# Performance work log

Measured on AMD Instinct MI355X. Metric: run time of the kernel, lower is better.

Reference implementation:

```python
import jax, jax.numpy as jnp
import numpy as np

EPS = 1e-5
GROUPS = 32


def setup_inputs() -> dict:
    key = jax.random.key(0)
    ks = jax.random.split(key, 3)
    B, C, H, W = 4, 256, 64, 64
    x = jax.random.normal(ks[0], (B, C, H, W), dtype=jnp.float32)
    gn_w = jnp.ones((C,), dtype=jnp.float32)
    gn_b = jnp.zeros((C,), dtype=jnp.float32)
    qkv_w = jax.random.normal(ks[1], (3 * C, C), dtype=jnp.float32) * (C ** -0.5)
    qkv_b = jnp.zeros((3 * C,), dtype=jnp.float32)
    proj_w = jax.random.normal(ks[2], (C, C), dtype=jnp.float32) * (C ** -0.5)
    proj_b = jnp.zeros((C,), dtype=jnp.float32)
    return {"x": x, "gn_w": gn_w, "gn_b": gn_b, "qkv_w": qkv_w,
            "qkv_b": qkv_b, "proj_w": proj_w, "proj_b": proj_b}


def reference(x, gn_w, gn_b, qkv_w, qkv_b, proj_w, proj_b):
    B, C, H, W = x.shape
    N = H * W
    # GroupNorm over (C//G, H, W) per group
    xg = x.reshape(B, GROUPS, -1)
    mean = xg.mean(axis=-1, keepdims=True)
    var = xg.var(axis=-1, keepdims=True)
    h = ((xg - mean) * jax.lax.rsqrt(var + EPS)).reshape(B, C, H, W)
    h = h * gn_w[None, :, None, None] + gn_b[None, :, None, None]
    # 1x1 conv QKV == channel GEMM
    hf = h.reshape(B, C, N)
    qkv = jnp.einsum('oc,bcn->bon', qkv_w, hf) + qkv_b[None, :, None]
    q, k, v = (qkv[:, :C], qkv[:, C:2 * C], qkv[:, 2 * C:])  # each [B,C,N]
    scale = C ** -0.5
    attn = jax.nn.softmax(jnp.einsum('bcn,bcm->bnm', q, k) * scale, axis=-1)
    out = jnp.einsum('bnm,bcm->bcn', attn, v)  # [B,C,N]
    y = jnp.einsum('oc,bcn->bon', proj_w, out) + proj_b[None, :, None]
    return x + y.reshape(B, C, H, W)
```

## Files before the change

kernel.cpp:

```cpp
#include <hip/hip_runtime.h>
#include <cstdint>
#include <cstddef>

typedef __attribute__((ext_vector_type(8))) short bf16x8;
typedef __attribute__((ext_vector_type(4))) short s16x4;
typedef __attribute__((ext_vector_type(2))) short s16x2;
typedef __attribute__((ext_vector_type(4))) float f32x4;
typedef __attribute__((ext_vector_type(16))) float f32x16;
typedef __attribute__((ext_vector_type(4))) unsigned u32x4;

#define DEVI static __device__ __forceinline__

DEVI short f2bf(float f){
  unsigned u = __builtin_bit_cast(unsigned, f);
  u += 0x7fffu + ((u >> 16) & 1u);
  return (short)(u >> 16);
}
DEVI float bf2f(short s){
  unsigned u = ((unsigned)(unsigned short)s) << 16;
  return __builtin_bit_cast(float, u);
}
DEVI unsigned pack_bf16_rne(float a, float b){
  unsigned ua = __builtin_bit_cast(unsigned, a);
  unsigned ub = __builtin_bit_cast(unsigned, b);
  ua += 0x7fffu + ((ua >> 16) & 1u);
  ub += 0x7fffu + ((ub >> 16) & 1u);
  return (ua >> 16) | (ub & 0xffff0000u);
}

DEVI f32x4 mfma16(bf16x8 a, bf16x8 b, f32x4 c){
  return __builtin_amdgcn_mfma_f32_16x16x32_bf16(a, b, c, 0, 0, 0);
}
DEVI f32x16 mfma32(bf16x8 a, bf16x8 b, f32x16 c){
  return __builtin_amdgcn_mfma_f32_32x32x16_bf16(a, b, c, 0, 0, 0);
}

#define QSC 0.09016844005555897f
#define FIXM 8.0f

__global__ __launch_bounds__(256) void k_stats(const float* __restrict__ x, float2* __restrict__ pst,
                                               const float* __restrict__ wq, const float* __restrict__ wp,
                                               short* __restrict__ wqb, short* __restrict__ wpb){
  if (blockIdx.x >= 512){
    int t = (blockIdx.x - 512) * 256 + threadIdx.x;
    for (int i = t; i < 768 * 256; i += 256 * 256) wqb[i] = f2bf(wq[i]);
    if (t < 256 * 256) wpb[t] = f2bf(wp[t]);
    return;
  }
  int blk = blockIdx.x;
  int b = blk >> 7, g = (blk >> 2) & 31, sub = blk & 3;
  const f32x4* p = (const f32x4*)(x + ((size_t)(b * 256 + g * 8)) * 4096) + sub * 2048;
  float s = 0.f, ss = 0.f;
  for (int i = threadIdx.x; i < 2048; i += 256){
    f32x4 v = p[i];
    s  += v[0] + v[1] + v[2] + v[3];
    ss += v[0]*v[0] + v[1]*v[1] + v[2]*v[2] + v[3]*v[3];
  }
  for (int d = 32; d; d >>= 1){ s += __shfl_down(s, d); ss += __shfl_down(ss, d); }
  __shared__ float a0[4], a1[4];
  int w = threadIdx.x >> 6;
  if ((threadIdx.x & 63) == 0){ a0[w] = s; a1[w] = ss; }
  __syncthreads();
  if (threadIdx.x == 0){
    s = a0[0] + a0[1] + a0[2] + a0[3];
    ss = a1[0] + a1[1] + a1[2] + a1[3];
    pst[blk] = make_float2(s, ss);
  }
}

__global__ __launch_bounds__(256) void k_norm(const float* __restrict__ x, const float2* __restrict__ pst,
                                              const float* __restrict__ gw, const float* __restrict__ gb,
                                              short* __restrict__ h_t){
  __shared__ short t[256][66];
  __shared__ float2 st_s[32];
  int b = blockIdx.x >> 6;
  int n0 = (blockIdx.x & 63) * 64;
  int tid = threadIdx.x;
  if (tid < 32){
    const float2* pp = pst + (b * 32 + tid) * 4;
    float2 q0 = pp[0], q1 = pp[1], q2 = pp[2], q3 = pp[3];
    float s = q0.x + q1.x + q2.x + q3.x;
    float ss = q0.y + q1.y + q2.y + q3.y;
    float mean = s * (1.f / 32768.f);
    float var = ss * (1.f / 32768.f) - mean * mean;
    st_s[tid] = make_float2(mean, rsqrtf(var + 1e-5f));
  }
  __syncthreads();
  for (int r = 0; r < 16; ++r){
    int idx = tid + r * 256;
    int c = idx >> 4, ch = idx & 15;
    f32x4 v = *(const f32x4*)(x + ((size_t)(b * 256 + c)) * 4096 + n0 + ch * 4);
    float2 s = st_s[c >> 3];
    float wv = gw[c] * s.y;
    float bv = gb[c] - s.x * wv;
    s16x2 p0, p1;
    p0[0] = f2bf(v[0] * wv + bv); p0[1] = f2bf(v[1] * wv + bv);
    p1[0] = f2bf(v[2] * wv + bv); p1[1] = f2bf(v[3] * wv + bv);
    *(s16x2*)&t[c][ch * 4]     = p0;
    *(s16x2*)&t[c][ch * 4 + 2] = p1;
  }
  __syncthreads();
  for (int r = 0; r < 8; ++r){
    int idx = tid + r * 256;
    int n = idx >> 5, cc = idx & 31;
    bf16x8 pk;
    #pragma unroll
    for (int j = 0; j < 8; ++j) pk[j] = t[cc * 8 + j][n];
    *(bf16x8*)(h_t + ((size_t)(b * 4096 + n0 + n)) * 256 + cc * 8) = pk;
  }
}

__global__ __launch_bounds__(256) void k_gemm(const short* __restrict__ A,
                                              const short* __restrict__ Bsrc,
                                              const float* __restrict__ bias,
                                              int mtiles, int mode,
                                              short* __restrict__ q_t, short* __restrict__ k_t,
                                              short* __restrict__ v_,
                                              const float* __restrict__ xres, float* __restrict__ outp)
{
  __shared__ short a_s[128 * 72];
  __shared__ short b_s[128 * 72];
  int t = blockIdx.x;
  int mt = t % mtiles; t /= mtiles;
  int nt = t & 31; int b = t >> 5;
  int o0 = mt * 128, n0 = nt * 128;
  int tid = threadIdx.x;
  int lane = tid & 63, w = tid >> 6;
  int col = lane & 15, quad = lane >> 4;
  int wo = (w >> 1) * 64, wn = (w & 1) * 64;

  f32x4 acc[4][4];
  #pragma unroll
  for (int i = 0; i < 4; ++i)
    #pragma unroll
    for (int j = 0; j < 4; ++j)
      #pragma unroll
      for (int r = 0; r < 4; ++r) acc[i][j][r] = 0.f;

  for (int kk = 0; kk < 4; ++kk){
    int k0 = kk * 64;
    #pragma unroll
    for (int r = 0; r < 4; ++r){
      int idx = tid + r * 256;
      int row = idx >> 3, ch = idx & 7;
      *(bf16x8*)&a_s[row * 72 + ch * 8] = *(const bf16x8*)(A + (size_t)(o0 + row) * 256 + k0 + ch * 8);
      *(bf16x8*)&b_s[row * 72 + ch * 8] = *(const bf16x8*)(Bsrc + ((size_t)(b * 4096 + n0 + row)) * 256 + k0 + ch * 8);
    }
    __syncthreads();
    #pragma unroll
    for (int kc = 0; kc < 2; ++kc){
      bf16x8 af[4], bfr[4];
      #pragma unroll
      for (int i = 0; i < 4; ++i) af[i]  = *(bf16x8*)&a_s[(wo + i * 16 + col) * 72 + kc * 32 + quad * 8];
      #pragma unroll
      for (int j = 0; j < 4; ++j) bfr[j] = *(bf16x8*)&b_s[(wn + j * 16 + col) * 72 + kc * 32 + quad * 8];
      #pragma unroll
      for (int i = 0; i < 4; ++i)
        #pragma unroll
        for (int j = 0; j < 4; ++j)
          acc[i][j] = mfma16(af[i], bfr[j], acc[i][j]);
    }
    __syncthreads();
  }

  float bv[4][4];
  #pragma unroll
  for (int i = 0; i < 4; ++i)
    #pragma unroll
    for (int r = 0; r < 4; ++r) bv[i][r] = bias[o0 + wo + i * 16 + quad * 4 + r];

  if (mode == 0){
    int region = o0 >> 8;
    int obase = (o0 & 255) + wo;
    if (region < 2){
      short* dst = region ? k_t : q_t;
      float sc = region ? 1.0f : QSC;
      #pragma unroll
      for (int i = 0; i < 4; ++i)
        #pragma unroll
        for (int j = 0; j < 4; ++j){
          int n = n0 + wn + j * 16 + col;
          s16x4 pk;
          #pragma unroll
          for (int r = 0; r < 4; ++r) pk[r] = f2bf((acc[i][j][r] + bv[i][r]) * sc);
          *(s16x4*)(dst + ((size_t)(b * 4096 + n)) * 256 + obase + i * 16 + quad * 4) = pk;
        }
    } else {
      #pragma unroll
      for (int i = 0; i < 4; ++i)
        #pragma unroll
        for (int r = 0; r < 4; ++r){
          int oo = obase + i * 16 + quad * 4 + r;
          #pragma unroll
          for (int j = 0; j < 4; ++j){
            int n = n0 + wn + j * 16 + col;
            v_[((size_t)(b * 256 + oo)) * 4096 + n] = f2bf(acc[i][j][r] + bv[i][r]);
          }
        }
    }
  } else {
    #pragma unroll
    for (int i = 0; i < 4; ++i)
      #pragma unroll
      for (int r = 0; r < 4; ++r){
        int oo = o0 + wo + i * 16 + quad * 4 + r;
        #pragma unroll
        for (int j = 0; j < 4; ++j){
          int n = n0 + wn + j * 16 + col;
          size_t off = ((size_t)(b * 256 + oo)) * 4096 + n;
          outp[off] = xres[off] + acc[i][j][r] + bv[i][r];
        }
      }
  }
}

__global__ __launch_bounds__(256, 2) void k_attn(const short* __restrict__ q_t, const short* __restrict__ k_t,
                                                 const short* __restrict__ v_,
                                                 short* __restrict__ o_part, float* __restrict__ lsum)
{
  __shared__ short k_s[32 * 256];
  __shared__ short v_s[256 * 32];
  int idx = blockIdx.x;
  int qt = idx >> 4;
  int chunk = idx & 15;
  int b  = chunk >> 2;
  int ck = chunk & 3;
  int q0 = qt * 128;
  int tid = threadIdx.x, lane = tid & 63, w = tid >> 6;
  int col = lane & 31, h = lane >> 5;

  const short* qp = q_t + ((size_t)(b * 4096 + q0 + w * 32 + col)) * 256 + h * 8;
  bf16x8 qf[16];
  #pragma unroll
  for (int ks2 = 0; ks2 < 16; ++ks2) qf[ks2] = *(const bf16x8*)(qp + ks2 * 16);

  const short* kcb = k_t + ((size_t)(b * 4096 + ck * 1024)) * 256;
  const short* vcb = v_  + ((size_t)b) * 256 * 4096 + ck * 1024;

  int k_r = w * 8 + (lane >> 5);
  int k_p = lane & 31;
  int v_c = w * 64 + (lane >> 2);
  int v_p = lane & 3;

  f32x16 o_acc[8];
  #pragma unroll
  for (int ct = 0; ct < 8; ++ct)
    #pragma unroll
    for (int r = 0; r < 16; ++r) o_acc[ct][r] = 0.f;
  float l_acc = 0.f;

  #pragma unroll 1
  for (int it = 0; it < 32; ++it){
    int m0 = it * 32;
    bf16x8 kst[4], vst[4];
    #pragma unroll
    for (int i = 0; i < 4; ++i){
      kst[i] = *(const bf16x8*)(kcb + (size_t)(m0 + k_r + i * 2) * 256 + k_p * 8);
      vst[i] = *(const bf16x8*)(vcb + (size_t)(v_c + i * 16) * 4096 + m0 + v_p * 8);
    }
    if (it) __syncthreads();
    #pragma unroll
    for (int i = 0; i < 4; ++i){
      int r = k_r + i * 2;
      *(bf16x8*)&k_s[r * 256 + (k_p ^ (r & 31)) * 8] = kst[i];
      int c = v_c + i * 16;
      *(bf16x8*)&v_s[c * 32 + (v_p ^ ((c >> 1) & 3)) * 8] = vst[i];
    }
    __syncthreads();

    f32x16 s;
    #pragma unroll
    for (int r = 0; r < 16; ++r) s[r] = 0.f;
    #pragma unroll
    for (int ks2 = 0; ks2 < 16; ++ks2){
      bf16x8 kb = *(const bf16x8*)&k_s[col * 256 + (((ks2 * 2 + h) ^ (col & 31)) * 8)];
      s = mfma32(kb, qf[ks2], s);
    }

    bf16x8 pa0, pa1;
    {
      float p0 = __builtin_amdgcn_exp2f(s[0] - FIXM);
      float p1 = __builtin_amdgcn_exp2f(s[1] - FIXM);
      float p2 = __builtin_amdgcn_exp2f(s[2] - FIXM);
      float p3 = __builtin_amdgcn_exp2f(s[3] - FIXM);
      float p4 = __builtin_amdgcn_exp2f(s[4] - FIXM);
      float p5 = __builtin_amdgcn_exp2f(s[5] - FIXM);
      float p6 = __builtin_amdgcn_exp2f(s[6] - FIXM);
      float p7 = __builtin_amdgcn_exp2f(s[7] - FIXM);
      l_acc += p0 + p1 + p2 + p3 + p4 + p5 + p6 + p7;
      unsigned A0 = pack_bf16_rne(p0, p1), A1 = pack_bf16_rne(p2, p3);
      unsigned B0 = pack_bf16_rne(p4, p5), B1 = pack_bf16_rne(p6, p7);
      asm volatile("v_permlane32_swap_b32 %0, %1" : "+v"(A0), "+v"(B0));
      asm volatile("v_permlane32_swap_b32 %0, %1" : "+v"(A1), "+v"(B1));
      u32x4 w0;
      w0[0] = A0;  w0[1] = A1;  w0[2] = B0;  w0[3] = B1;
      pa0 = __builtin_bit_cast(bf16x8, w0);
    }
    {
      float p0 = __builtin_amdgcn_exp2f(s[8]  - FIXM);
      float p1 = __builtin_amdgcn_exp2f(s[9]  - FIXM);
      float p2 = __builtin_amdgcn_exp2f(s[10] - FIXM);
      float p3 = __builtin_amdgcn_exp2f(s[11] - FIXM);
      float p4 = __builtin_amdgcn_exp2f(s[12] - FIXM);
      float p5 = __builtin_amdgcn_exp2f(s[13] - FIXM);
      float p6 = __builtin_amdgcn_exp2f(s[14] - FIXM);
      float p7 = __builtin_amdgcn_exp2f(s[15] - FIXM);
      l_acc += p0 + p1 + p2 + p3 + p4 + p5 + p6 + p7;
      unsigned C0 = pack_bf16_rne(p0, p1), C1 = pack_bf16_rne(p2, p3);
      unsigned D0 = pack_bf16_rne(p4, p5), D1 = pack_bf16_rne(p6, p7);
      asm volatile("v_permlane32_swap_b32 %0, %1" : "+v"(C0), "+v"(D0));
      asm volatile("v_permlane32_swap_b32 %0, %1" : "+v"(C1), "+v"(D1));
      u32x4 w1;
      w1[0] = C0;  w1[1] = C1;  w1[2] = D0;  w1[3] = D1;
      pa1 = __builtin_bit_cast(bf16x8, w1);
    }

    #pragma unroll
    for (int ct = 0; ct < 8; ++ct){
      int c = ct * 32 + col;
      int sw = (c >> 1) & 3;
      bf16x8 vf0 = *(const bf16x8*)&v_s[c * 32 + ((h ^ sw) * 8)];
      bf16x8 vf1 = *(const bf16x8*)&v_s[c * 32 + (((2 + h) ^ sw) * 8)];
      o_acc[ct] = mfma32(pa0, vf0, o_acc[ct]);
      o_acc[ct] = mfma32(pa1, vf1, o_acc[ct]);
    }
  }

  short* op = o_part + (((size_t)(ck * 4 + b)) * 4096 + q0 + w * 32) * 256;
  #pragma unroll
  for (int r = 0; r < 16; ++r){
    int q = (r & 3) + 8 * (r >> 2) + 4 * h;
    #pragma unroll
    for (int ct = 0; ct < 8; ++ct)
      op[(size_t)q * 256 + ct * 32 + col] = f2bf(o_acc[ct][r]);
  }
  l_acc += __shfl_xor(l_acc, 32);
  if (h == 0)
    lsum[((size_t)(ck * 4 + b)) * 4096 + q0 + w * 32 + col] = l_acc;
}

__global__ __launch_bounds__(256) void k_comb(const short* __restrict__ o_part, const float* __restrict__ lsum,
                                              short* __restrict__ o_t)
{
  int t = blockIdx.x * 256 + threadIdx.x;
  int row = t >> 5;
  int c8 = (t & 31) * 8;
  float inv = 1.f / (lsum[row] + lsum[16384 + row] + lsum[2 * 16384 + row] + lsum[3 * 16384 + row]);
  size_t base = (size_t)row * 256 + c8;
  const size_t CS = (size_t)16384 * 256;
  bf16x8 a0 = *(const bf16x8*)(o_part + base);
  bf16x8 a1 = *(const bf16x8*)(o_part + CS + base);
  bf16x8 a2 = *(const bf16x8*)(o_part + 2 * CS + base);
  bf16x8 a3 = *(const bf16x8*)(o_part + 3 * CS + base);
  bf16x8 outv;
  #pragma unroll
  for (int j = 0; j < 8; ++j)
    outv[j] = f2bf((bf2f(a0[j]) + bf2f(a1[j]) + bf2f(a2[j]) + bf2f(a3[j])) * inv);
  *(bf16x8*)(o_t + base) = outv;
}

extern "C" void kernel_launch(void* const* d_in, const int* in_sizes, int n_in,
                              void* d_out, int out_size, void* d_ws, size_t ws_size,
                              hipStream_t stream)
{
  const float* x     = (const float*)d_in[0];
  const float* gw    = (const float*)d_in[1];
  const float* gb    = (const float*)d_in[2];
  const float* qkvw  = (const float*)d_in[3];
  const float* qkvb  = (const float*)d_in[4];
  const float* projw = (const float*)d_in[5];
  const float* projb = (const float*)d_in[6];
  float* out = (float*)d_out;

  char* ws = (char*)d_ws;
  float2* pst = (float2*)ws;
  short* wqb = (short*)(ws + 4096);
  short* wpb = (short*)(ws + 4096 + 393216);
  short* h_t = (short*)(ws + 4096 + 393216 + 131072);
  const size_t BIG = (size_t)4 * 4096 * 256;
  short* q_t = h_t + BIG;
  short* k_t = q_t + BIG;
  short* v_  = k_t + BIG;
  short* o_t = v_  + BIG;
  short* o_part = o_t + BIG;
  float* lsum = (float*)(o_part + 4 * BIG);

  k_stats<<<dim3(768),  dim3(256), 0, stream>>>(x, pst, qkvw, projw, wqb, wpb);
  k_norm <<<dim3(256),  dim3(256), 0, stream>>>(x, pst, gw, gb, h_t);
  k_gemm <<<dim3(768),  dim3(256), 0, stream>>>(wqb, h_t, qkvb, 6, 0, q_t, k_t, v_,
                                                (const float*)nullptr, (float*)nullptr);
  k_attn <<<dim3(512),  dim3(256), 0, stream>>>(q_t, k_t, v_, o_part, lsum);
  k_comb <<<dim3(2048), dim3(256), 0, stream>>>(o_part, lsum, o_t);
  k_gemm <<<dim3(256),  dim3(256), 0, stream>>>(wpb, o_t, projb, 2, 1,
                                                (short*)nullptr, (short*)nullptr, (short*)nullptr,
                                                x, out);
}
```

Baseline: 197.0 us.

## Fuse split-K attention combine into projection GEMM loads; retune V LDS swizzle

```diff
diff --git a/kernel.cpp b/kernel.cpp
--- a/kernel.cpp
+++ b/kernel.cpp
@@ -116,7 +116,8 @@
                                               int mtiles, int mode,
                                               short* __restrict__ q_t, short* __restrict__ k_t,
                                               short* __restrict__ v_,
-                                              const float* __restrict__ xres, float* __restrict__ outp)
+                                              const float* __restrict__ xres, float* __restrict__ outp,
+                                              const float* __restrict__ lsum)
 {
   __shared__ short a_s[128 * 72];
   __shared__ short b_s[128 * 72];
@@ -144,7 +145,23 @@
       int idx = tid + r * 256;
       int row = idx >> 3, ch = idx & 7;
       *(bf16x8*)&a_s[row * 72 + ch * 8] = *(const bf16x8*)(A + (size_t)(o0 + row) * 256 + k0 + ch * 8);
-      *(bf16x8*)&b_s[row * 72 + ch * 8] = *(const bf16x8*)(Bsrc + ((size_t)(b * 4096 + n0 + row)) * 256 + k0 + ch * 8);
+      if (mode == 0){
+        *(bf16x8*)&b_s[row * 72 + ch * 8] = *(const bf16x8*)(Bsrc + ((size_t)(b * 4096 + n0 + row)) * 256 + k0 + ch * 8);
+      } else {
+        const size_t CS = (size_t)16384 * 256;
+        int grow = b * 4096 + n0 + row;
+        size_t base = (size_t)grow * 256 + k0 + ch * 8;
+        bf16x8 c0 = *(const bf16x8*)(Bsrc + base);
+        bf16x8 c1 = *(const bf16x8*)(Bsrc + CS + base);
+        bf16x8 c2 = *(const bf16x8*)(Bsrc + 2 * CS + base);
+        bf16x8 c3 = *(const bf16x8*)(Bsrc + 3 * CS + base);
+        float inv = 1.f / (lsum[grow] + lsum[16384 + grow] + lsum[2 * 16384 + grow] + lsum[3 * 16384 + grow]);
+        bf16x8 pk;
+        #pragma unroll
+        for (int j = 0; j < 8; ++j)
+          pk[j] = f2bf((bf2f(c0[j]) + bf2f(c1[j]) + bf2f(c2[j]) + bf2f(c3[j])) * inv);
+        *(bf16x8*)&b_s[row * 72 + ch * 8] = pk;
+      }
     }
     __syncthreads();
     #pragma unroll
@@ -264,7 +281,7 @@
       int r = k_r + i * 2;
       *(bf16x8*)&k_s[r * 256 + (k_p ^ (r & 31)) * 8] = kst[i];
       int c = v_c + i * 16;
-      *(bf16x8*)&v_s[c * 32 + (v_p ^ ((c >> 1) & 3)) * 8] = vst[i];
+      *(bf16x8*)&v_s[c * 32 + (v_p ^ ((c >> 3) & 3)) * 8] = vst[i];
     }
     __syncthreads();
 
@@ -318,7 +335,7 @@
     #pragma unroll
     for (int ct = 0; ct < 8; ++ct){
       int c = ct * 32 + col;
-      int sw = (c >> 1) & 3;
+      int sw = (c >> 3) & 3;
       bf16x8 vf0 = *(const bf16x8*)&v_s[c * 32 + ((h ^ sw) * 8)];
       bf16x8 vf1 = *(const bf16x8*)&v_s[c * 32 + (((2 + h) ^ sw) * 8)];
       o_acc[ct] = mfma32(pa0, vf0, o_acc[ct]);
@@ -337,26 +354,6 @@
   l_acc += __shfl_xor(l_acc, 32);
   if (h == 0)
     lsum[((size_t)(ck * 4 + b)) * 4096 + q0 + w * 32 + col] = l_acc;
-}
-
-__global__ __launch_bounds__(256) void k_comb(const short* __restrict__ o_part, const float* __restrict__ lsum,
-                                              short* __restrict__ o_t)
-{
-  int t = blockIdx.x * 256 + threadIdx.x;
-  int row = t >> 5;
-  int c8 = (t & 31) * 8;
-  float inv = 1.f / (lsum[row] + lsum[16384 + row] + lsum[2 * 16384 + row] + lsum[3 * 16384 + row]);
-  size_t base = (size_t)row * 256 + c8;
-  const size_t CS = (size_t)16384 * 256;
-  bf16x8 a0 = *(const bf16x8*)(o_part + base);
-  bf16x8 a1 = *(const bf16x8*)(o_part + CS + base);
-  bf16x8 a2 = *(const bf16x8*)(o_part + 2 * CS + base);
-  bf16x8 a3 = *(const bf16x8*)(o_part + 3 * CS + base);
-  bf16x8 outv;
-  #pragma unroll
-  for (int j = 0; j < 8; ++j)
-    outv[j] = f2bf((bf2f(a0[j]) + bf2f(a1[j]) + bf2f(a2[j]) + bf2f(a3[j])) * inv);
-  *(bf16x8*)(o_t + base) = outv;
 }
 
 extern "C" void kernel_launch(void* const* d_in, const int* in_sizes, int n_in,
@@ -381,17 +378,16 @@
   short* q_t = h_t + BIG;
   short* k_t = q_t + BIG;
   short* v_  = k_t + BIG;
-  short* o_t = v_  + BIG;
-  short* o_part = o_t + BIG;
+  short* o_part = v_ + BIG;
   float* lsum = (float*)(o_part + 4 * BIG);
 
   k_stats<<<dim3(768),  dim3(256), 0, stream>>>(x, pst, qkvw, projw, wqb, wpb);
   k_norm <<<dim3(256),  dim3(256), 0, stream>>>(x, pst, gw, gb, h_t);
   k_gemm <<<dim3(768),  dim3(256), 0, stream>>>(wqb, h_t, qkvb, 6, 0, q_t, k_t, v_,
-                                                (const float*)nullptr, (float*)nullptr);
+                                                (const float*)nullptr, (float*)nullptr,
+                                                (const float*)nullptr);
   k_attn <<<dim3(512),  dim3(256), 0, stream>>>(q_t, k_t, v_, o_part, lsum);
-  k_comb <<<dim3(2048), dim3(256), 0, stream>>>(o_part, lsum, o_t);
-  k_gemm <<<dim3(256),  dim3(256), 0, stream>>>(wpb, o_t, projb, 2, 1,
+  k_gemm <<<dim3(256),  dim3(256), 0, stream>>>(wpb, o_part, projb, 2, 1,
                                                 (short*)nullptr, (short*)nullptr, (short*)nullptr,
-                                                x, out);
-}
+                                                x, out, lsum);
+}
```

Result: slower. 214.6 us (+9.0%).
